# Optimization experiments

Hardware: AMD Instinct MI355X
Metric: run time of the kernel (lower is better)

## Reference

```python
import jax, jax.numpy as jnp
import numpy as np

N_ATOMS = 256
N_FEATURES = 128
BATCH = 8
BINS = 300


def _segments(n, length=1):
    # all pairs of non-overlapping length-`length` segments: rows [i, i+L, j, j+L], j >= i+L+1
    m = n - length
    i, j = np.triu_indices(m, k=length + 1)
    return np.stack([i, i + length, j, j + length], axis=1).astype(np.int32)  # (Nseg, 4)


SEGMENTS_NP = _segments(N_ATOMS)
NSEG = SEGMENTS_NP.shape[0]  # 32131 for n_atoms=256
# edges: segment start-pairs and end-pairs, shape (2, 2*Nseg), then offset per frame
_edges_base = np.concatenate([SEGMENTS_NP[:, [0, 2]], SEGMENTS_NP[:, [1, 3]]], axis=0).T
EDGES_NP = np.concatenate([b * N_ATOMS + _edges_base for b in range(BATCH)], axis=1)  # (2, B*2*Nseg)
SRC = jnp.asarray(EDGES_NP[0].astype(np.int32))
DST = jnp.asarray(EDGES_NP[1].astype(np.int32))
SEGMENTS = jnp.asarray(SEGMENTS_NP)
BIN_CENTERS = jnp.linspace(-1.0, 1.0, BINS, dtype=jnp.float32)
STEP = 2.0 / (BINS - 1)  # linear (non-gaussian) binning: scalar step


def _divnorm(x):
    return x / jnp.linalg.norm(x, axis=-1, keepdims=True)


def _writhe_segments_cross(xyz, seg):
    # xyz: (B, N, 3), seg: (S, 4) -> writhe per segment pair (B, S)
    B, S = xyz.shape[0], seg.shape[0]
    # dx[b, s, k]: broadcasted differences xyz[seg[2+q]] - xyz[seg[p]], k = 2*p+q
    dx = (-xyz[:, seg[:, :2], None] + xyz[:, seg[:, None, 2:]]).reshape(B, S, 4, 3)
    dx = _divnorm(dx)
    crosses = _divnorm(jnp.cross(dx[:, :, [0, 1, 3, 2]], dx[:, :, [1, 3, 2, 0]]))
    dots = jnp.clip(jnp.sum(crosses * crosses[:, :, [1, 2, 3, 0]], axis=-1), -1.0, 1.0)
    omega = jnp.arcsin(dots).sum(axis=2)  # (B, S)
    signs = jnp.sign(jnp.sum(
        jnp.cross(xyz[:, seg[:, 3]] - xyz[:, seg[:, 2]], xyz[:, seg[:, 1]] - xyz[:, seg[:, 0]]) * dx[:, :, 0],
        axis=-1))
    return omega * signs / (2.0 * jnp.pi)


def setup_inputs() -> dict:
    key = jax.random.key(0)
    k1, k2, k3 = jax.random.split(key, 3)
    coords = jax.random.normal(k1, (BATCH * N_ATOMS, 3), jnp.float32)
    node_features = jax.random.normal(k2, (BATCH * N_ATOMS, N_FEATURES), jnp.float32)
    std = 1.0 / np.sqrt(N_FEATURES)
    basis = jax.random.uniform(k3, (BINS, N_FEATURES), jnp.float32, -std, std)
    return {"coords": coords, "node_features": node_features, "basis": basis}


def reference(coords, node_features, basis):
    xyz = coords.reshape(BATCH, N_ATOMS, 3)
    wr = _writhe_segments_cross(xyz, SEGMENTS)  # (B, Nseg)
    # Gaussian RBF soft one-hot over linear bins, then project onto learned basis
    enc = jnp.exp(-(((wr[..., None] - BIN_CENTERS) / STEP) ** 2)) / 1.12  # (B, S, bins)
    emb = jnp.einsum('bsk,kf->bsf', enc, basis)  # (B, S, F)
    # repeat(1,2,1): each segment pair contributes two edges (start-pair, end-pair)
    writhe_feat = jnp.tile(emb, (1, 2, 1)).reshape(-1, N_FEATURES)  # (B*2S, F)
    # distance attention: exp(-||r_src - r_dst||^2), softmax-normalized per destination node
    w = jnp.exp(-jnp.sum((coords[SRC] - coords[DST]) ** 2, axis=-1))  # (E,)
    denom = jax.ops.segment_sum(w, DST, num_segments=BATCH * N_ATOMS)
    attn = (w / denom[DST])[:, None]
    message = jax.ops.segment_sum(writhe_feat * attn, DST, num_segments=BATCH * N_ATOMS)
    return node_features + message
```

## Files before the change

### kernel.cpp

```cpp
#include <hip/hip_runtime.h>
#include <math.h>

#define N_ATOMS 256
#define N_FEAT  128
#define BATCH   8
#define BINS    300
#define INV_STEP 149.5f
#define ONE_OVER_2PI 0.15915494309189535f
#define INV_112 0.8928571428571429f
#define WIN 6
#define WINW 13
#define NHIST 8

struct V3 { float x, y, z; };
__device__ __forceinline__ V3 v3sub(V3 a, V3 b) { return {a.x-b.x, a.y-b.y, a.z-b.z}; }
__device__ __forceinline__ float v3dot(V3 a, V3 b) { return a.x*b.x + a.y*b.y + a.z*b.z; }
__device__ __forceinline__ V3 v3cross(V3 a, V3 b) {
    return {a.y*b.z - a.z*b.y, a.z*b.x - a.x*b.z, a.x*b.y - a.y*b.x};
}
__device__ __forceinline__ V3 v3nrm(V3 a) {
    float r = __builtin_amdgcn_rsqf(v3dot(a, a));
    return {a.x*r, a.y*r, a.z*r};
}
__device__ __forceinline__ float clamp1(float x) { return fminf(1.0f, fmaxf(-1.0f, x)); }

__device__ __forceinline__ float asin_fast(float x) {
    float u = fabsf(x);
    bool big = u > 0.5f;
    float z = big ? 0.5f * (1.0f - u) : u * u;
    float s = big ? __builtin_amdgcn_sqrtf(z) : u;
    float p = fmaf(z, 4.2163199048e-2f, 2.4181311049e-2f);
    p = fmaf(z, p, 4.5470025998e-2f);
    p = fmaf(z, p, 7.4953002686e-2f);
    p = fmaf(z, p, 1.6666752422e-1f);
    float r = fmaf(s * z, p, s);
    r = big ? (1.5707963267948966f - 2.0f * r) : r;
    return copysignf(r, x);
}

__device__ __forceinline__ float writhe_ij(const float* cs, int i, int j) {
    V3 pi  = {cs[i*3+0],     cs[i*3+1],     cs[i*3+2]};
    V3 pi1 = {cs[(i+1)*3+0], cs[(i+1)*3+1], cs[(i+1)*3+2]};
    V3 pj  = {cs[j*3+0],     cs[j*3+1],     cs[j*3+2]};
    V3 pj1 = {cs[(j+1)*3+0], cs[(j+1)*3+1], cs[(j+1)*3+2]};

    V3 d0 = v3nrm(v3sub(pj,  pi));
    V3 d1 = v3nrm(v3sub(pj1, pi));
    V3 d2 = v3nrm(v3sub(pj,  pi1));
    V3 d3 = v3nrm(v3sub(pj1, pi1));

    V3 c0 = v3nrm(v3cross(d0, d1));
    V3 c1 = v3nrm(v3cross(d1, d3));
    V3 c2 = v3nrm(v3cross(d3, d2));
    V3 c3 = v3nrm(v3cross(d2, d0));

    float omega = asin_fast(clamp1(v3dot(c0, c1)))
                + asin_fast(clamp1(v3dot(c1, c2)))
                + asin_fast(clamp1(v3dot(c2, c3)))
                + asin_fast(clamp1(v3dot(c3, c0)));

    float sg = v3dot(v3cross(v3sub(pj1, pj), v3sub(pi1, pi)), d0);
    float sign = (sg > 0.0f) ? 1.0f : ((sg < 0.0f) ? -1.0f : 0.0f);
    return omega * sign * ONE_OVER_2PI;
}

__global__ __launch_bounds__(512) void fused_kernel(const float* __restrict__ coords,
                                                    const float* __restrict__ nf,
                                                    const float* __restrict__ basis,
                                                    float* __restrict__ out) {
    const int blk = blockIdx.x;
    const int b = blk & 7;
    const int t = blk >> 3;
    const int n = (b << 8) | t;
    const int tid = threadIdx.x;

    float mynf = 0.0f;
    if (tid < N_FEAT) mynf = nf[(size_t)n * N_FEAT + tid];

    if (t < 2) {
        if (tid < N_FEAT) out[(size_t)n * N_FEAT + tid] = mynf;
        return;
    }

    __shared__ float cs[N_ATOMS * 3];
    __shared__ float h8[NHIST * BINS];
    __shared__ float part4[4 * N_FEAT];
    __shared__ float sden;
    __shared__ int skmin, skmax;

    for (int idx = tid; idx < N_ATOMS * 3; idx += 512)
        cs[idx] = coords[(b << 8) * 3 + idx];
    for (int k = tid; k < NHIST * BINS; k += 512) h8[k] = 0.0f;
    if (tid == 0) { sden = 0.0f; skmin = BINS - 1; skmax = 0; }
    __syncthreads();

    const bool e1 = (t <= N_ATOMS - 2);
    const int typ = tid >> 8;
    const int a = tid & 255;
    const bool active = (a <= t - 2) && (typ == 0 ? e1 : (a >= 1));

    float dsum = 0.0f;
    int kminl = BINS - 1, kmaxl = 0;

    if (active) {
        float dx = cs[a*3+0] - cs[t*3+0];
        float dy = cs[a*3+1] - cs[t*3+1];
        float dz = cs[a*3+2] - cs[t*3+2];
        float g = __expf(-(dx*dx + dy*dy + dz*dz));
        dsum = g;

        float w = (typ == 0) ? writhe_ij(cs, a, t) : writhe_ij(cs, a - 1, t - 1);
        float p = (w + 1.0f) * INV_STEP;
        int k0 = __float2int_rn(p);
        kminl = max(0, k0 - WIN);
        kmaxl = min(BINS - 1, k0 + WIN);

        const int copy = tid & (NHIST - 1);
        const int rot = tid % WINW;
        int klo = k0 - WIN;
        #pragma unroll
        for (int m = 0; m < WINW; ++m) {
            int mm = m + rot; if (mm >= WINW) mm -= WINW;
            int k = klo + mm;
            if (k >= 0 && k < BINS) {
                float d = p - (float)k;
                atomicAdd(&h8[copy * BINS + k], g * __expf(-d * d));
            }
        }
    }

    #pragma unroll
    for (int off = 32; off > 0; off >>= 1) {
        dsum += __shfl_xor(dsum, off, 64);
        kminl = min(kminl, __shfl_xor(kminl, off, 64));
        kmaxl = max(kmaxl, __shfl_xor(kmaxl, off, 64));
    }
    if ((tid & 63) == 0) {
        atomicAdd(&sden, dsum);
        atomicMin(&skmin, kminl);
        atomicMax(&skmax, kmaxl);
    }
    __syncthreads();

    const int kmin = skmin;
    const int kmax = skmax;
    for (int k = kmin + tid; k <= kmax; k += 512) {
        float s = h8[k];
        #pragma unroll
        for (int c = 1; c < NHIST; ++c) s += h8[c * BINS + k];
        h8[k] = s;
    }
    __syncthreads();

    const int len = kmax - kmin + 1;
    const int chunk = (len + 3) >> 2;
    const int q = tid >> 7;
    const int f = tid & (N_FEAT - 1);
    int ks = kmin + q * chunk;
    int ke = min(ks + chunk, kmin + len);
    float acc = 0.0f;
    for (int k = ks; k < ke; ++k)
        acc = fmaf(h8[k], basis[k * N_FEAT + f], acc);
    part4[q * N_FEAT + f] = acc;
    __syncthreads();

    if (tid < N_FEAT) {
        float s = part4[tid] + part4[N_FEAT + tid]
                + part4[2 * N_FEAT + tid] + part4[3 * N_FEAT + tid];
        out[(size_t)n * N_FEAT + tid] = mynf + s * (INV_112 / sden);
    }
}

extern "C" void kernel_launch(void* const* d_in, const int* in_sizes, int n_in,
                              void* d_out, int out_size, void* d_ws, size_t ws_size,
                              hipStream_t stream) {
    const float* coords = (const float*)d_in[0];
    const float* nf     = (const float*)d_in[1];
    const float* basis  = (const float*)d_in[2];
    float* out = (float*)d_out;

    fused_kernel<<<BATCH * N_ATOMS, 512, 0, stream>>>(coords, nf, basis, out);
}
```

Before: 122.7 us.

## Pair short and long destination nodes per block and narrow RBF window

Each block now handles two destination nodes, t0=p+2 and t1=255-p, so that their incoming edge counts add up to about 512 and fill all threads. This balances work across blocks and halves the grid. Separate histograms, denominators and bin ranges are kept for each node, and nodes 0 and 1 are copied by the p==0 blocks. The Gaussian RBF window is also cut from ±6 to ±2 bins, which drops contributions the truncated exp(-d²) still counted before and so trades accuracy for fewer shared-memory atomics.

```diff
diff --git a/kernel.cpp b/kernel.cpp
--- a/kernel.cpp
+++ b/kernel.cpp
@@ -8,8 +8,8 @@
 #define INV_STEP 149.5f
 #define ONE_OVER_2PI 0.15915494309189535f
 #define INV_112 0.8928571428571429f
-#define WIN 6
-#define WINW 13
+#define WIN 2
+#define WINW 5
 #define NHIST 8
 
 struct V3 { float x, y, z; };
@@ -70,104 +70,136 @@
                                                     float* __restrict__ out) {
     const int blk = blockIdx.x;
     const int b = blk & 7;
-    const int t = blk >> 3;
-    const int n = (b << 8) | t;
+    const int p = blk >> 3;
+    const int t0 = p + 2;
+    const int t1 = 255 - p;
     const int tid = threadIdx.x;
 
+    const int E0  = 2 * t0 - 3;
+    const int E1n = (t1 == 255) ? 253 : 2 * t1 - 3;
+
     float mynf = 0.0f;
-    if (tid < N_FEAT) mynf = nf[(size_t)n * N_FEAT + tid];
-
-    if (t < 2) {
-        if (tid < N_FEAT) out[(size_t)n * N_FEAT + tid] = mynf;
-        return;
+    if (tid < 256) {
+        const int row = (tid >> 7) ? t1 : t0;
+        mynf = nf[((size_t)((b << 8) | row)) * N_FEAT + (tid & 127)];
     }
 
     __shared__ float cs[N_ATOMS * 3];
-    __shared__ float h8[NHIST * BINS];
-    __shared__ float part4[4 * N_FEAT];
-    __shared__ float sden;
-    __shared__ int skmin, skmax;
+    __shared__ float h2[2 * NHIST * BINS];
+    __shared__ float part[4 * N_FEAT];
+    __shared__ float sden[2];
+    __shared__ int skmin[2], skmax[2];
 
     for (int idx = tid; idx < N_ATOMS * 3; idx += 512)
         cs[idx] = coords[(b << 8) * 3 + idx];
-    for (int k = tid; k < NHIST * BINS; k += 512) h8[k] = 0.0f;
-    if (tid == 0) { sden = 0.0f; skmin = BINS - 1; skmax = 0; }
-    __syncthreads();
-
-    const bool e1 = (t <= N_ATOMS - 2);
-    const int typ = tid >> 8;
-    const int a = tid & 255;
-    const bool active = (a <= t - 2) && (typ == 0 ? e1 : (a >= 1));
-
-    float dsum = 0.0f;
-    int kminl = BINS - 1, kmaxl = 0;
-
-    if (active) {
-        float dx = cs[a*3+0] - cs[t*3+0];
-        float dy = cs[a*3+1] - cs[t*3+1];
-        float dz = cs[a*3+2] - cs[t*3+2];
+    for (int k = tid; k < 2 * NHIST * BINS; k += 512) h2[k] = 0.0f;
+    if (tid < 2) { sden[tid] = 0.0f; skmin[tid] = BINS - 1; skmax[tid] = 0; }
+    __syncthreads();
+
+    int node = -1;
+    int tau = t0;
+    if (tid < E0) { node = 0; tau = t0; }
+    else if (tid < E0 + E1n) { node = 1; tau = t1; }
+    const int ee = (node == 1) ? tid - E0 : tid;
+
+    float d0 = 0.0f, d1 = 0.0f;
+    int kn0 = BINS - 1, kx0 = 0, kn1 = BINS - 1, kx1 = 0;
+
+    if (node >= 0) {
+        const int eT1 = (tau <= N_ATOMS - 2) ? tau - 1 : 0;
+        const int typ = (ee < eT1) ? 0 : 1;
+        const int a = (typ == 0) ? ee : ee - eT1 + 1;
+
+        float dx = cs[a*3+0] - cs[tau*3+0];
+        float dy = cs[a*3+1] - cs[tau*3+1];
+        float dz = cs[a*3+2] - cs[tau*3+2];
         float g = __expf(-(dx*dx + dy*dy + dz*dz));
-        dsum = g;
-
-        float w = (typ == 0) ? writhe_ij(cs, a, t) : writhe_ij(cs, a - 1, t - 1);
-        float p = (w + 1.0f) * INV_STEP;
-        int k0 = __float2int_rn(p);
-        kminl = max(0, k0 - WIN);
-        kmaxl = min(BINS - 1, k0 + WIN);
+
+        float w = (typ == 0) ? writhe_ij(cs, a, tau) : writhe_ij(cs, a - 1, tau - 1);
+        float pp = (w + 1.0f) * INV_STEP;
+        int k0 = __float2int_rn(pp);
+        int kmn = max(0, k0 - WIN);
+        int kmx = min(BINS - 1, k0 + WIN);
+        if (node == 0) { d0 = g; kn0 = kmn; kx0 = kmx; }
+        else           { d1 = g; kn1 = kmn; kx1 = kmx; }
 
         const int copy = tid & (NHIST - 1);
         const int rot = tid % WINW;
-        int klo = k0 - WIN;
+        const int base = (node * NHIST + copy) * BINS;
+        const int klo = k0 - WIN;
         #pragma unroll
         for (int m = 0; m < WINW; ++m) {
             int mm = m + rot; if (mm >= WINW) mm -= WINW;
             int k = klo + mm;
             if (k >= 0 && k < BINS) {
-                float d = p - (float)k;
-                atomicAdd(&h8[copy * BINS + k], g * __expf(-d * d));
+                float dd = pp - (float)k;
+                atomicAdd(&h2[base + k], g * __expf(-dd * dd));
             }
         }
     }
 
     #pragma unroll
     for (int off = 32; off > 0; off >>= 1) {
-        dsum += __shfl_xor(dsum, off, 64);
-        kminl = min(kminl, __shfl_xor(kminl, off, 64));
-        kmaxl = max(kmaxl, __shfl_xor(kmaxl, off, 64));
+        d0 += __shfl_xor(d0, off, 64);
+        d1 += __shfl_xor(d1, off, 64);
+        kn0 = min(kn0, __shfl_xor(kn0, off, 64));
+        kx0 = max(kx0, __shfl_xor(kx0, off, 64));
+        kn1 = min(kn1, __shfl_xor(kn1, off, 64));
+        kx1 = max(kx1, __shfl_xor(kx1, off, 64));
     }
     if ((tid & 63) == 0) {
-        atomicAdd(&sden, dsum);
-        atomicMin(&skmin, kminl);
-        atomicMax(&skmax, kmaxl);
-    }
-    __syncthreads();
-
-    const int kmin = skmin;
-    const int kmax = skmax;
-    for (int k = kmin + tid; k <= kmax; k += 512) {
-        float s = h8[k];
-        #pragma unroll
-        for (int c = 1; c < NHIST; ++c) s += h8[c * BINS + k];
-        h8[k] = s;
-    }
-    __syncthreads();
-
-    const int len = kmax - kmin + 1;
-    const int chunk = (len + 3) >> 2;
-    const int q = tid >> 7;
-    const int f = tid & (N_FEAT - 1);
-    int ks = kmin + q * chunk;
-    int ke = min(ks + chunk, kmin + len);
-    float acc = 0.0f;
-    for (int k = ks; k < ke; ++k)
-        acc = fmaf(h8[k], basis[k * N_FEAT + f], acc);
-    part4[q * N_FEAT + f] = acc;
-    __syncthreads();
-
-    if (tid < N_FEAT) {
-        float s = part4[tid] + part4[N_FEAT + tid]
-                + part4[2 * N_FEAT + tid] + part4[3 * N_FEAT + tid];
-        out[(size_t)n * N_FEAT + tid] = mynf + s * (INV_112 / sden);
+        atomicAdd(&sden[0], d0);
+        atomicAdd(&sden[1], d1);
+        atomicMin(&skmin[0], kn0);
+        atomicMax(&skmax[0], kx0);
+        atomicMin(&skmin[1], kn1);
+        atomicMax(&skmax[1], kx1);
+    }
+    __syncthreads();
+
+    {
+        const int nu = tid >> 8;
+        const int kmin = skmin[nu], kmax = skmax[nu];
+        const int base = nu * NHIST * BINS;
+        for (int k = kmin + (tid & 255); k <= kmax; k += 256) {
+            float s = h2[base + k];
+            #pragma unroll
+            for (int c = 1; c < NHIST; ++c) s += h2[base + c * BINS + k];
+            h2[base + k] = s;
+        }
+    }
+    __syncthreads();
+
+    {
+        const int nu = tid >> 8;
+        const int h = (tid >> 7) & 1;
+        const int f = tid & 127;
+        const int kmin = skmin[nu], kmax = skmax[nu];
+        const int len = kmax - kmin + 1;
+        const int half = (len + 1) >> 1;
+        const int ks = kmin + h * half;
+        const int ke = min(kmax + 1, ks + half);
+        const int base = nu * NHIST * BINS;
+        float acc = 0.0f;
+        for (int k = ks; k < ke; ++k)
+            acc = fmaf(h2[base + k], basis[k * N_FEAT + f], acc);
+        part[((nu << 1) | h) * N_FEAT + f] = acc;
+    }
+    __syncthreads();
+
+    if (tid < 256) {
+        const int nu = tid >> 7;
+        const int f = tid & 127;
+        const int row = nu ? t1 : t0;
+        const float scale = INV_112 / sden[nu];
+        const float s = part[(nu << 1) * N_FEAT + f] + part[((nu << 1) | 1) * N_FEAT + f];
+        out[((size_t)((b << 8) | row)) * N_FEAT + f] = mynf + s * scale;
+    } else if (p == 0) {
+        const int tid2 = tid - 256;
+        const int r = tid2 >> 7;
+        const int f = tid2 & 127;
+        const size_t idx = ((size_t)((b << 8) | r)) * N_FEAT + f;
+        out[idx] = nf[idx];
     }
 }
 
@@ -179,5 +211,5 @@
     const float* basis  = (const float*)d_in[2];
     float* out = (float*)d_out;
 
-    fused_kernel<<<BATCH * N_ATOMS, 512, 0, stream>>>(coords, nf, basis, out);
-}
+    fused_kernel<<<BATCH * 127, 512, 0, stream>>>(coords, nf, basis, out);
+}
```

Measured after the change: 104.9 us. -14.5%, faster.
